# Kernel tuning notes

Measured on AMD Instinct MI355X. Metric: run time of the kernel, lower is better.

## Reference

```python
import jax, jax.numpy as jnp
import numpy as np

IN_F, OUT_F, R = 4096, 4096, 16
SCALING = 32.0 / R  # lora_alpha / r


def setup_inputs() -> dict:
    key = jax.random.key(0)
    kx, kw, kb, ka, kB = jax.random.split(key, 5)
    bound_w = 1.0 / np.sqrt(IN_F)  # kaiming_uniform a=sqrt(5) on (out,in) -> U(-1/sqrt(in), 1/sqrt(in))
    x = jax.random.normal(kx, (4, 4096, IN_F), dtype=jnp.float32)
    weight = jax.random.uniform(kw, (OUT_F, IN_F), jnp.float32, -bound_w, bound_w)
    bias = jax.random.uniform(kb, (OUT_F,), jnp.float32, -bound_w, bound_w)
    lora_A = jax.random.uniform(ka, (R, IN_F), jnp.float32, -bound_w, bound_w)
    # B is zero-init in the module; use small random values so the LoRA path is exercised
    lora_B = jax.random.normal(kB, (OUT_F, R), dtype=jnp.float32) * 0.01
    return {"x": x, "weight": weight, "bias": bias, "lora_A": lora_A, "lora_B": lora_B}


def reference(x, weight, bias, lora_A, lora_B):
    # base: F.linear(x, W, b) = x @ W.T + b
    base_out = jnp.einsum("bsi,oi->bso", x, weight) + bias
    # low-rank path: (x @ A.T) @ B.T * scaling  (dropout=0 -> identity)
    xr = jnp.einsum("bsi,ri->bsr", x, lora_A)  # [b, s, r]
    lora_out = jnp.einsum("bsr,or->bso", xr, lora_B) * SCALING
    return base_out + lora_out
```

## Files before the change

### kernel.cpp

```cpp
#include <hip/hip_runtime.h>
#include <hip/hip_bf16.h>


typedef __attribute__((ext_vector_type(8))) short bf16x8;
typedef __attribute__((ext_vector_type(4))) float f32x4;
typedef __attribute__((ext_vector_type(4))) unsigned short u16x4;

#define M_DIM 16384
#define N_DIM 4096
#define K_DIM 4096
#define NT (K_DIM / 64)

__device__ __forceinline__ unsigned short f2bf(float f) {
    unsigned int u = __builtin_bit_cast(unsigned int, f);
    unsigned int r = u + 0x7FFFu + ((u >> 16) & 1u);
    return (unsigned short)(r >> 16);
}

__device__ __forceinline__ void async16(const void* g, void* l) {
    __builtin_amdgcn_global_load_lds(
        (const __attribute__((address_space(1))) unsigned int*)g,
        (__attribute__((address_space(3))) unsigned int*)l,
        16, 0, 0);
}

__global__ void __launch_bounds__(256) cast_x_kernel(
    const float4* __restrict__ x, u16x4* __restrict__ y, int n4) {
    int i = blockIdx.x * blockDim.x + threadIdx.x;
    int stride = gridDim.x * blockDim.x;
    for (; i < n4; i += stride) {
        float4 v = x[i];
        u16x4 o = { f2bf(v.x), f2bf(v.y), f2bf(v.z), f2bf(v.w) };
        y[i] = o;
    }
}

__global__ void __launch_bounds__(256) weff_kernel(
    const float* __restrict__ W, const float* __restrict__ lA,
    const float* __restrict__ lB, unsigned short* __restrict__ out) {
    constexpr int K = K_DIM, R = 16;
    constexpr float S = 2.0f;
    int o = blockIdx.x;
    int t = threadIdx.x;
    float b[R];
#pragma unroll
    for (int r = 0; r < R; ++r) b[r] = lB[o * R + r];
#pragma unroll
    for (int c = 0; c < 4; ++c) {
        int i = c * 1024 + t * 4;
        float4 wv = *reinterpret_cast<const float4*>(&W[o * K + i]);
        float sx = 0.f, sy = 0.f, sz = 0.f, sw = 0.f;
#pragma unroll
        for (int r = 0; r < R; ++r) {
            float4 a = *reinterpret_cast<const float4*>(&lA[r * K + i]);
            sx += b[r] * a.x; sy += b[r] * a.y;
            sz += b[r] * a.z; sw += b[r] * a.w;
        }
        u16x4 ov = { f2bf(wv.x + S * sx), f2bf(wv.y + S * sy),
                     f2bf(wv.z + S * sz), f2bf(wv.w + S * sw) };
        *reinterpret_cast<u16x4*>(&out[o * K + i]) = ov;
    }
}

#define STAGE(G, h, tt, bsel, moff)                                           \
    do {                                                                      \
        const unsigned short* g0 = (G) +                                      \
            (size_t)((h) * 128 + wid * 16 + rc) * K_DIM + (tt) * 64 + cc * 8; \
        char* l0 = lds + (bsel) * 65536 + (moff) + (h) * 16384 + wid * 2048;  \
        async16(g0, l0);                                                      \
        async16(g0 + 8 * K_DIM, l0 + 1024);                                   \
    } while (0)

#define LDA(mh, bsel)                                                         \
    _Pragma("unroll") for (int mm = 0; mm < 4; ++mm)                          \
    _Pragma("unroll") for (int ks = 0; ks < 2; ++ks)                          \
        ar[mm][ks] = *(const bf16x8*)(lds + (bsel) * 65536 +                  \
            ((aBase + ((mh) * 4 + mm) * 2048) ^ (ks << 6)));

#define LDB(nh, bsel)                                                         \
    _Pragma("unroll") for (int nn = 0; nn < 2; ++nn)                          \
    _Pragma("unroll") for (int ks = 0; ks < 2; ++ks)                          \
        br[(nh) * 2 + nn][ks] = *(const bf16x8*)(lds + (bsel) * 65536 +       \
            ((bBase + ((nh) * 2 + nn) * 2048) ^ (ks << 6)));

#define MM(mh, nh)                                                            \
    _Pragma("unroll") for (int ks = 0; ks < 2; ++ks)                          \
    _Pragma("unroll") for (int mm = 0; mm < 4; ++mm)                          \
    _Pragma("unroll") for (int nn = 0; nn < 2; ++nn)                          \
        acc[(mh) * 4 + mm][(nh) * 2 + nn] =                                   \
            __builtin_amdgcn_mfma_f32_16x16x32_bf16(                          \
                ar[mm][ks], br[(nh) * 2 + nn][ks],                            \
                acc[(mh) * 4 + mm][(nh) * 2 + nn], 0, 0, 0);

#define PHASE_MID()                                                           \
    __builtin_amdgcn_s_barrier();                                             \
    asm volatile("s_waitcnt lgkmcnt(0)" ::: "memory");                        \
    __builtin_amdgcn_s_setprio(1)

#define PHASE_END()                                                           \
    __builtin_amdgcn_s_setprio(0);                                            \
    __builtin_amdgcn_s_barrier()

__global__ void __launch_bounds__(512, 2) gemm8p_kernel(
    const unsigned short* __restrict__ A,
    const unsigned short* __restrict__ B,
    const float* __restrict__ bias,
    float* __restrict__ C) {
    __shared__ __align__(1024) char lds[131072];

    const int tid = threadIdx.x;
    const int lane = tid & 63, wid = tid >> 6;
    const int wm = wid >> 2, wn = wid & 3;
    const int lr = lane & 15, lg = lane >> 4;

    const int bid = blockIdx.x;
    const int swz = (bid & 7) * 128 + (bid >> 3);
    const int bm = swz >> 4, bn = swz & 15;

    const unsigned short* Ag = A + (size_t)bm * 256 * K_DIM;
    const unsigned short* Bg = B + (size_t)bn * 256 * K_DIM;

    const int lam = lane ^ (lane >> 3);
    const int rc = lam >> 3, cc = lam & 7;

    const int kx0 = (lg * 16) ^ ((lr & 7) << 4);
    const int aBase = (wm * 128 + lr) * 128 + kx0;
    const int bBase = 32768 + (wn * 64 + lr) * 128 + kx0;

    f32x4 acc[8][4] = {};
    bf16x8 ar[4][2], br[4][2];

    STAGE(Bg, 0, 0, 0, 32768);
    STAGE(Bg, 1, 0, 0, 32768);
    STAGE(Ag, 0, 0, 0, 0);
    STAGE(Ag, 1, 0, 0, 0);
    STAGE(Bg, 0, 1, 1, 32768);
    STAGE(Bg, 1, 1, 1, 32768);
    asm volatile("s_waitcnt vmcnt(4)" ::: "memory");
    __builtin_amdgcn_s_barrier();

#pragma unroll 2
    for (int t = 0; t < NT; ++t) {
        const int bs = t & 1, bo = bs ^ 1;
        LDA(0, bs);
        LDB(0, bs);
        if (t + 1 < NT) STAGE(Ag, 0, t + 1, bo, 0);
        PHASE_MID();
        MM(0, 0);
        PHASE_END();
        LDB(1, bs);
        if (t + 1 < NT) STAGE(Ag, 1, t + 1, bo, 0);
        PHASE_MID();
        MM(0, 1);
        PHASE_END();
        LDA(1, bs);
        if (t + 2 < NT) STAGE(Bg, 0, t + 2, bs, 32768);
        PHASE_MID();
        MM(1, 0);
        PHASE_END();
        if (t + 2 < NT) STAGE(Bg, 1, t + 2, bs, 32768);
        PHASE_MID();
        MM(1, 1);
        __builtin_amdgcn_s_setprio(0);
        if (t + 2 < NT) {
            asm volatile("s_waitcnt vmcnt(4)" ::: "memory");
        } else {
            asm volatile("s_waitcnt vmcnt(0)" ::: "memory");
        }
        __builtin_amdgcn_s_barrier();
    }

    const int row0 = bm * 256 + wm * 128;
    const int col0 = bn * 256 + wn * 64;
#pragma unroll
    for (int n = 0; n < 4; ++n) {
        const int col = col0 + n * 16 + lr;
        const float bv = bias[col];
#pragma unroll
        for (int m = 0; m < 8; ++m) {
            const int r0 = row0 + m * 16 + lg * 4;
#pragma unroll
            for (int r = 0; r < 4; ++r)
                C[(size_t)(r0 + r) * N_DIM + col] = acc[m][n][r] + bv;
        }
    }
}

extern "C" void kernel_launch(void* const* d_in, const int* in_sizes, int n_in,
                              void* d_out, int out_size, void* d_ws, size_t ws_size,
                              hipStream_t stream) {
    const float* x    = (const float*)d_in[0];
    const float* W    = (const float*)d_in[1];
    const float* bias = (const float*)d_in[2];
    const float* lA   = (const float*)d_in[3];
    const float* lB   = (const float*)d_in[4];
    float* out = (float*)d_out;

    unsigned short* xb   = (unsigned short*)d_ws;
    unsigned short* weff = (unsigned short*)((char*)d_ws + 134217728);

    cast_x_kernel<<<2048, 256, 0, stream>>>((const float4*)x, (u16x4*)xb,
                                            M_DIM * K_DIM / 4);
    weff_kernel<<<N_DIM, 256, 0, stream>>>(W, lA, lB, weff);
    gemm8p_kernel<<<(M_DIM / 256) * (N_DIM / 256), 512, 0, stream>>>(
        xb, weff, bias, out);
}
```

Measured before the change: 604.4 us.

## Switch GEMM inner loop to 32x32x16 bf16 MFMA and drop phase barriers

Replaces the 16x16x32 MFMA tiling with 32x32x16 bf16 MFMA instructions. Each wave now holds 4x2 tiles of 32x32 accumulators, and LDS fragment loads and swizzle offsets are recomputed for the new operand layout. Larger MFMA tiles need fewer LDS reads per flop and fewer instructions. Two of the four per-phase end barriers are also removed, cutting synchronisation. The trade-off is higher register pressure and a different LDS access pattern, and the reduced barriers could risk races on buffer reuse.

```diff
diff --git a/kernel.cpp b/kernel.cpp
--- a/kernel.cpp
+++ b/kernel.cpp
@@ -3,7 +3,7 @@
 
 
 typedef __attribute__((ext_vector_type(8))) short bf16x8;
-typedef __attribute__((ext_vector_type(4))) float f32x4;
+typedef __attribute__((ext_vector_type(16))) float f32x16;
 typedef __attribute__((ext_vector_type(4))) unsigned short u16x4;
 
 #define M_DIM 16384
@@ -71,35 +71,27 @@
         async16(g0 + 8 * K_DIM, l0 + 1024);                                   \
     } while (0)
 
-#define LDA(mh, bsel)                                                         \
-    _Pragma("unroll") for (int mm = 0; mm < 4; ++mm)                          \
-    _Pragma("unroll") for (int ks = 0; ks < 2; ++ks)                          \
-        ar[mm][ks] = *(const bf16x8*)(lds + (bsel) * 65536 +                  \
-            ((aBase + ((mh) * 4 + mm) * 2048) ^ (ks << 6)));
-
-#define LDB(nh, bsel)                                                         \
-    _Pragma("unroll") for (int nn = 0; nn < 2; ++nn)                          \
-    _Pragma("unroll") for (int ks = 0; ks < 2; ++ks)                          \
-        br[(nh) * 2 + nn][ks] = *(const bf16x8*)(lds + (bsel) * 65536 +       \
-            ((bBase + ((nh) * 2 + nn) * 2048) ^ (ks << 6)));
-
-#define MM(mh, nh)                                                            \
-    _Pragma("unroll") for (int ks = 0; ks < 2; ++ks)                          \
-    _Pragma("unroll") for (int mm = 0; mm < 4; ++mm)                          \
-    _Pragma("unroll") for (int nn = 0; nn < 2; ++nn)                          \
-        acc[(mh) * 4 + mm][(nh) * 2 + nn] =                                   \
-            __builtin_amdgcn_mfma_f32_16x16x32_bf16(                          \
-                ar[mm][ks], br[(nh) * 2 + nn][ks],                            \
-                acc[(mh) * 4 + mm][(nh) * 2 + nn], 0, 0, 0);
+#define LDA32(mh, bsel)                                                       \
+    _Pragma("unroll") for (int mm = 0; mm < 2; ++mm)                          \
+    _Pragma("unroll") for (int ks = 0; ks < 4; ++ks)                          \
+        ar[mm][ks] = *(const bf16x8*)(lds + (bsel) * 65536 + aoff +           \
+            ((mh) * 2 + mm) * 4096 + kx[ks]);
+
+#define LDB32(nh, bsel)                                                       \
+    _Pragma("unroll") for (int ks = 0; ks < 4; ++ks)                          \
+        br[nh][ks] = *(const bf16x8*)(lds + (bsel) * 65536 + boff +           \
+            (nh) * 4096 + kx[ks]);
+
+#define MM32(mh, nh)                                                          \
+    _Pragma("unroll") for (int ks = 0; ks < 4; ++ks)                          \
+    _Pragma("unroll") for (int mm = 0; mm < 2; ++mm)                          \
+        acc[(mh) * 2 + mm][nh] = __builtin_amdgcn_mfma_f32_32x32x16_bf16(     \
+            ar[mm][ks], br[nh][ks], acc[(mh) * 2 + mm][nh], 0, 0, 0);
 
 #define PHASE_MID()                                                           \
     __builtin_amdgcn_s_barrier();                                             \
     asm volatile("s_waitcnt lgkmcnt(0)" ::: "memory");                        \
     __builtin_amdgcn_s_setprio(1)
-
-#define PHASE_END()                                                           \
-    __builtin_amdgcn_s_setprio(0);                                            \
-    __builtin_amdgcn_s_barrier()
 
 __global__ void __launch_bounds__(512, 2) gemm8p_kernel(
     const unsigned short* __restrict__ A,
@@ -111,7 +103,7 @@
     const int tid = threadIdx.x;
     const int lane = tid & 63, wid = tid >> 6;
     const int wm = wid >> 2, wn = wid & 3;
-    const int lr = lane & 15, lg = lane >> 4;
+    const int lc = lane & 31, hi = lane >> 5;
 
     const int bid = blockIdx.x;
     const int swz = (bid & 7) * 128 + (bid >> 3);
@@ -123,12 +115,15 @@
     const int lam = lane ^ (lane >> 3);
     const int rc = lam >> 3, cc = lam & 7;
 
-    const int kx0 = (lg * 16) ^ ((lr & 7) << 4);
-    const int aBase = (wm * 128 + lr) * 128 + kx0;
-    const int bBase = 32768 + (wn * 64 + lr) * 128 + kx0;
-
-    f32x4 acc[8][4] = {};
-    bf16x8 ar[4][2], br[4][2];
+    const int sw = (lane & 7) << 4;
+    int kx[4];
+#pragma unroll
+    for (int ks = 0; ks < 4; ++ks) kx[ks] = ((ks << 5) | (hi << 4)) ^ sw;
+    const int aoff = (wm * 128 + lc) * 128;
+    const int boff = 32768 + (wn * 64 + lc) * 128;
+
+    f32x16 acc[4][2] = {};
+    bf16x8 ar[2][4], br[2][4];
 
     STAGE(Bg, 0, 0, 0, 32768);
     STAGE(Bg, 1, 0, 0, 32768);
@@ -142,25 +137,26 @@
 #pragma unroll 2
     for (int t = 0; t < NT; ++t) {
         const int bs = t & 1, bo = bs ^ 1;
-        LDA(0, bs);
-        LDB(0, bs);
+        LDA32(0, bs);
+        LDB32(0, bs);
         if (t + 1 < NT) STAGE(Ag, 0, t + 1, bo, 0);
         PHASE_MID();
-        MM(0, 0);
-        PHASE_END();
-        LDB(1, bs);
+        MM32(0, 0);
+        __builtin_amdgcn_s_setprio(0);
+        LDB32(1, bs);
         if (t + 1 < NT) STAGE(Ag, 1, t + 1, bo, 0);
         PHASE_MID();
-        MM(0, 1);
-        PHASE_END();
-        LDA(1, bs);
+        MM32(0, 1);
+        __builtin_amdgcn_s_setprio(0);
+        __builtin_amdgcn_s_barrier();
+        LDA32(1, bs);
         if (t + 2 < NT) STAGE(Bg, 0, t + 2, bs, 32768);
         PHASE_MID();
-        MM(1, 0);
-        PHASE_END();
+        MM32(1, 0);
+        __builtin_amdgcn_s_setprio(0);
         if (t + 2 < NT) STAGE(Bg, 1, t + 2, bs, 32768);
         PHASE_MID();
-        MM(1, 1);
+        MM32(1, 1);
         __builtin_amdgcn_s_setprio(0);
         if (t + 2 < NT) {
             asm volatile("s_waitcnt vmcnt(4)" ::: "memory");
@@ -173,15 +169,19 @@
     const int row0 = bm * 256 + wm * 128;
     const int col0 = bn * 256 + wn * 64;
 #pragma unroll
-    for (int n = 0; n < 4; ++n) {
-        const int col = col0 + n * 16 + lr;
+    for (int n = 0; n < 2; ++n) {
+        const int col = col0 + n * 32 + lc;
         const float bv = bias[col];
 #pragma unroll
-        for (int m = 0; m < 8; ++m) {
-            const int r0 = row0 + m * 16 + lg * 4;
-#pragma unroll
-            for (int r = 0; r < 4; ++r)
-                C[(size_t)(r0 + r) * N_DIM + col] = acc[m][n][r] + bv;
+        for (int m = 0; m < 4; ++m) {
+#pragma unroll
+            for (int g = 0; g < 4; ++g) {
+#pragma unroll
+                for (int r = 0; r < 4; ++r) {
+                    const int row = row0 + m * 32 + g * 8 + 4 * hi + r;
+                    C[(size_t)row * N_DIM + col] = acc[m][n][g * 4 + r] + bv;
+                }
+            }
         }
     }
 }
```

Result: slower. 643.8 us (+6.5%).

## Make GEMM persistent over four tiles with cross-tile prefetch and fewer barriers

Applied to the files above, without the earlier changes.

The GEMM grid shrinks from 1024 blocks to 256, and each block walks a 2x2 group of 256x256 output tiles in a snake order. Loads for the next tile are issued during the last iterations of the current tile, so the pipeline does not drain and refill between tiles. Two of the four per-iteration barriers are also removed. The intent is to cut per-block prologue/epilogue cost, tail imbalance and barrier overhead. The risks are a single wave of 256 blocks leaving some CUs idle and races from the removed barriers.

```diff
diff --git a/kernel.cpp b/kernel.cpp
--- a/kernel.cpp
+++ b/kernel.cpp
@@ -9,7 +9,7 @@
 #define M_DIM 16384
 #define N_DIM 4096
 #define K_DIM 4096
-#define NT (K_DIM / 64)
+#define NT 64
 
 __device__ __forceinline__ unsigned short f2bf(float f) {
     unsigned int u = __builtin_bit_cast(unsigned int, f);
@@ -97,10 +97,6 @@
     asm volatile("s_waitcnt lgkmcnt(0)" ::: "memory");                        \
     __builtin_amdgcn_s_setprio(1)
 
-#define PHASE_END()                                                           \
-    __builtin_amdgcn_s_setprio(0);                                            \
-    __builtin_amdgcn_s_barrier()
-
 __global__ void __launch_bounds__(512, 2) gemm8p_kernel(
     const unsigned short* __restrict__ A,
     const unsigned short* __restrict__ B,
@@ -114,11 +110,16 @@
     const int lr = lane & 15, lg = lane >> 4;
 
     const int bid = blockIdx.x;
-    const int swz = (bid & 7) * 128 + (bid >> 3);
-    const int bm = swz >> 4, bn = swz & 15;
-
-    const unsigned short* Ag = A + (size_t)bm * 256 * K_DIM;
-    const unsigned short* Bg = B + (size_t)bn * 256 * K_DIM;
+    const int qm = bid >> 3, qn = bid & 7;
+    const int bmArr[4] = { 2 * qm, 2 * qm, 2 * qm + 1, 2 * qm + 1 };
+    const int bnArr[4] = { 2 * qn, 2 * qn + 1, 2 * qn + 1, 2 * qn };
+    const unsigned short* AgArr[4];
+    const unsigned short* BgArr[4];
+#pragma unroll
+    for (int i = 0; i < 4; ++i) {
+        AgArr[i] = A + (size_t)bmArr[i] * 256 * K_DIM;
+        BgArr[i] = B + (size_t)bnArr[i] * 256 * K_DIM;
+    }
 
     const int lam = lane ^ (lane >> 3);
     const int rc = lam >> 3, cc = lam & 7;
@@ -127,61 +128,78 @@
     const int aBase = (wm * 128 + lr) * 128 + kx0;
     const int bBase = 32768 + (wn * 64 + lr) * 128 + kx0;
 
-    f32x4 acc[8][4] = {};
     bf16x8 ar[4][2], br[4][2];
 
-    STAGE(Bg, 0, 0, 0, 32768);
-    STAGE(Bg, 1, 0, 0, 32768);
-    STAGE(Ag, 0, 0, 0, 0);
-    STAGE(Ag, 1, 0, 0, 0);
-    STAGE(Bg, 0, 1, 1, 32768);
-    STAGE(Bg, 1, 1, 1, 32768);
+    STAGE(BgArr[0], 0, 0, 0, 32768);
+    STAGE(BgArr[0], 1, 0, 0, 32768);
+    STAGE(AgArr[0], 0, 0, 0, 0);
+    STAGE(AgArr[0], 1, 0, 0, 0);
+    STAGE(BgArr[0], 0, 1, 1, 32768);
+    STAGE(BgArr[0], 1, 1, 1, 32768);
     asm volatile("s_waitcnt vmcnt(4)" ::: "memory");
     __builtin_amdgcn_s_barrier();
 
+#pragma unroll
+    for (int tau = 0; tau < 4; ++tau) {
+        const int nx = (tau < 3) ? tau + 1 : 3;
+        const unsigned short* AgC = AgArr[tau];
+        const unsigned short* AgN = AgArr[nx];
+        const unsigned short* BgC = BgArr[tau];
+        const unsigned short* BgN = BgArr[nx];
+
+        f32x4 acc[8][4] = {};
+
 #pragma unroll 2
-    for (int t = 0; t < NT; ++t) {
-        const int bs = t & 1, bo = bs ^ 1;
-        LDA(0, bs);
-        LDB(0, bs);
-        if (t + 1 < NT) STAGE(Ag, 0, t + 1, bo, 0);
-        PHASE_MID();
-        MM(0, 0);
-        PHASE_END();
-        LDB(1, bs);
-        if (t + 1 < NT) STAGE(Ag, 1, t + 1, bo, 0);
-        PHASE_MID();
-        MM(0, 1);
-        PHASE_END();
-        LDA(1, bs);
-        if (t + 2 < NT) STAGE(Bg, 0, t + 2, bs, 32768);
-        PHASE_MID();
-        MM(1, 0);
-        PHASE_END();
-        if (t + 2 < NT) STAGE(Bg, 1, t + 2, bs, 32768);
-        PHASE_MID();
-        MM(1, 1);
-        __builtin_amdgcn_s_setprio(0);
-        if (t + 2 < NT) {
-            asm volatile("s_waitcnt vmcnt(4)" ::: "memory");
-        } else {
-            asm volatile("s_waitcnt vmcnt(0)" ::: "memory");
+        for (int t = 0; t < NT; ++t) {
+            const int bs = t & 1, bo = bs ^ 1;
+            const unsigned short* As = (t < NT - 1) ? AgC : AgN;
+            const unsigned short* Bs = (t < NT - 2) ? BgC : BgN;
+            const int ta = (t + 1) & 63;
+            const int tb = (t + 2) & 63;
+            const bool doA = (tau < 3) || (t < NT - 1);
+            const bool doB = (tau < 3) || (t < NT - 2);
+            LDA(0, bs);
+            LDB(0, bs);
+            if (doA) STAGE(As, 0, ta, bo, 0);
+            PHASE_MID();
+            MM(0, 0);
+            __builtin_amdgcn_s_setprio(0);
+            LDB(1, bs);
+            if (doA) STAGE(As, 1, ta, bo, 0);
+            PHASE_MID();
+            MM(0, 1);
+            __builtin_amdgcn_s_setprio(0);
+            __builtin_amdgcn_s_barrier();
+            LDA(1, bs);
+            if (doB) STAGE(Bs, 0, tb, bs, 32768);
+            PHASE_MID();
+            MM(1, 0);
+            __builtin_amdgcn_s_setprio(0);
+            if (doB) STAGE(Bs, 1, tb, bs, 32768);
+            PHASE_MID();
+            MM(1, 1);
+            __builtin_amdgcn_s_setprio(0);
+            if (doB) {
+                asm volatile("s_waitcnt vmcnt(4)" ::: "memory");
+            } else {
+                asm volatile("s_waitcnt vmcnt(0)" ::: "memory");
+            }
+            __builtin_amdgcn_s_barrier();
         }
-        __builtin_amdgcn_s_barrier();
-    }
-
-    const int row0 = bm * 256 + wm * 128;
-    const int col0 = bn * 256 + wn * 64;
-#pragma unroll
-    for (int n = 0; n < 4; ++n) {
-        const int col = col0 + n * 16 + lr;
-        const float bv = bias[col];
-#pragma unroll
-        for (int m = 0; m < 8; ++m) {
-            const int r0 = row0 + m * 16 + lg * 4;
-#pragma unroll
-            for (int r = 0; r < 4; ++r)
-                C[(size_t)(r0 + r) * N_DIM + col] = acc[m][n][r] + bv;
+
+        const int row0 = bmArr[tau] * 256 + wm * 128;
+        const int col0 = bnArr[tau] * 256 + wn * 64;
+#pragma unroll
+        for (int n = 0; n < 4; ++n) {
+            const int col = col0 + n * 16 + lr;
+            const float bv = bias[col];
+#pragma unroll
+            for (int m = 0; m < 8; ++m) {
+                const int r0 = row0 + m * 16 + lg * 4;
+#pragma unroll
+                for (int r = 0; r < 4; ++r)
+                    C[(size_t)(r0 + r) * N_DIM + col] = acc[m][n][r] + bv;
+            }
         }
     }
 }
@@ -202,6 +220,5 @@
     cast_x_kernel<<<2048, 256, 0, stream>>>((const float4*)x, (u16x4*)xb,
                                             M_DIM * K_DIM / 4);
     weff_kernel<<<N_DIM, 256, 0, stream>>>(W, lA, lB, weff);
-    gemm8p_kernel<<<(M_DIM / 256) * (N_DIM / 256), 512, 0, stream>>>(
-        xb, weff, bias, out);
-}
+    gemm8p_kernel<<<256, 512, 0, stream>>>(xb, weff, bias, out);
+}
```

After: 682.3 us. 12.9% more time.

## Cut GEMM main-loop barriers from eight to two with double-buffered A fragments

Applied to the files above, without the earlier changes.

Restructures the bf16 GEMM inner loop so that all B fragments and the first A half are loaded up front, both A-tile async stages are issued together, and the second A half goes into a separate register set while the first MFMA quarter runs. This removes most of the per-phase barriers and explicit lgkmcnt waits, leaving one mid-loop barrier and one end barrier per iteration, with MFMA priority raised around each quarter. The aim is to cut synchronisation stalls and let LDS reads overlap MFMA work. In exchange it uses more registers, and it relies on compiler-inserted waits to keep the async B refill from overwriting LDS that is still being read.

```diff
diff --git a/kernel.cpp b/kernel.cpp
--- a/kernel.cpp
+++ b/kernel.cpp
@@ -9,7 +9,7 @@
 #define M_DIM 16384
 #define N_DIM 4096
 #define K_DIM 4096
-#define NT (K_DIM / 64)
+#define NT 64
 
 __device__ __forceinline__ unsigned short f2bf(float f) {
     unsigned int u = __builtin_bit_cast(unsigned int, f);
@@ -71,37 +71,32 @@
         async16(g0 + 8 * K_DIM, l0 + 1024);                                   \
     } while (0)
 
-#define LDA(mh, bsel)                                                         \
+#define LDA_TO(dst, mh, bsel)                                                 \
     _Pragma("unroll") for (int mm = 0; mm < 4; ++mm)                          \
     _Pragma("unroll") for (int ks = 0; ks < 2; ++ks)                          \
-        ar[mm][ks] = *(const bf16x8*)(lds + (bsel) * 65536 +                  \
+        dst[mm][ks] = *(const bf16x8*)(lds + (bsel) * 65536 +                 \
             ((aBase + ((mh) * 4 + mm) * 2048) ^ (ks << 6)));
 
-#define LDB(nh, bsel)                                                         \
+#define LDB_TO(nh, bsel)                                                      \
     _Pragma("unroll") for (int nn = 0; nn < 2; ++nn)                          \
     _Pragma("unroll") for (int ks = 0; ks < 2; ++ks)                          \
         br[(nh) * 2 + nn][ks] = *(const bf16x8*)(lds + (bsel) * 65536 +       \
             ((bBase + ((nh) * 2 + nn) * 2048) ^ (ks << 6)));
 
-#define MM(mh, nh)                                                            \
+#define MM_Q(src, mh, nh)                                                     \
+    __builtin_amdgcn_s_setprio(1);                                            \
     _Pragma("unroll") for (int ks = 0; ks < 2; ++ks)                          \
     _Pragma("unroll") for (int mm = 0; mm < 4; ++mm)                          \
     _Pragma("unroll") for (int nn = 0; nn < 2; ++nn)                          \
         acc[(mh) * 4 + mm][(nh) * 2 + nn] =                                   \
             __builtin_amdgcn_mfma_f32_16x16x32_bf16(                          \
-                ar[mm][ks], br[(nh) * 2 + nn][ks],                            \
-                acc[(mh) * 4 + mm][(nh) * 2 + nn], 0, 0, 0);
-
-#define PHASE_MID()                                                           \
-    __builtin_amdgcn_s_barrier();                                             \
-    asm volatile("s_waitcnt lgkmcnt(0)" ::: "memory");                        \
-    __builtin_amdgcn_s_setprio(1)
-
-#define PHASE_END()                                                           \
-    __builtin_amdgcn_s_setprio(0);                                            \
-    __builtin_amdgcn_s_barrier()
-
-__global__ void __launch_bounds__(512, 2) gemm8p_kernel(
+                src[mm][ks], br[(nh) * 2 + nn][ks],                           \
+                acc[(mh) * 4 + mm][(nh) * 2 + nn], 0, 0, 0);                  \
+    __builtin_amdgcn_s_setprio(0)
+
+#define CFENCE() asm volatile("" ::: "memory")
+
+__global__ void __launch_bounds__(512, 2) gemm2b_kernel(
     const unsigned short* __restrict__ A,
     const unsigned short* __restrict__ B,
     const float* __restrict__ bias,
@@ -128,7 +123,7 @@
     const int bBase = 32768 + (wn * 64 + lr) * 128 + kx0;
 
     f32x4 acc[8][4] = {};
-    bf16x8 ar[4][2], br[4][2];
+    bf16x8 arA[4][2], arB[4][2], br[4][2];
 
     STAGE(Bg, 0, 0, 0, 32768);
     STAGE(Bg, 1, 0, 0, 32768);
@@ -138,36 +133,35 @@
     STAGE(Bg, 1, 1, 1, 32768);
     asm volatile("s_waitcnt vmcnt(4)" ::: "memory");
     __builtin_amdgcn_s_barrier();
+    CFENCE();
 
 #pragma unroll 2
     for (int t = 0; t < NT; ++t) {
         const int bs = t & 1, bo = bs ^ 1;
-        LDA(0, bs);
-        LDB(0, bs);
-        if (t + 1 < NT) STAGE(Ag, 0, t + 1, bo, 0);
-        PHASE_MID();
-        MM(0, 0);
-        PHASE_END();
-        LDB(1, bs);
-        if (t + 1 < NT) STAGE(Ag, 1, t + 1, bo, 0);
-        PHASE_MID();
-        MM(0, 1);
-        PHASE_END();
-        LDA(1, bs);
+        LDA_TO(arA, 0, bs);
+        LDB_TO(0, bs);
+        LDB_TO(1, bs);
+        if (t + 1 < NT) {
+            STAGE(Ag, 0, t + 1, bo, 0);
+            STAGE(Ag, 1, t + 1, bo, 0);
+        }
+        MM_Q(arA, 0, 0);
+        LDA_TO(arB, 1, bs);
+        MM_Q(arA, 0, 1);
+        CFENCE();
+        __builtin_amdgcn_s_barrier();
+        CFENCE();
         if (t + 2 < NT) STAGE(Bg, 0, t + 2, bs, 32768);
-        PHASE_MID();
-        MM(1, 0);
-        PHASE_END();
+        MM_Q(arB, 1, 0);
         if (t + 2 < NT) STAGE(Bg, 1, t + 2, bs, 32768);
-        PHASE_MID();
-        MM(1, 1);
-        __builtin_amdgcn_s_setprio(0);
-        if (t + 2 < NT) {
+        MM_Q(arB, 1, 1);
+        if (t < NT - 2) {
             asm volatile("s_waitcnt vmcnt(4)" ::: "memory");
         } else {
             asm volatile("s_waitcnt vmcnt(0)" ::: "memory");
         }
         __builtin_amdgcn_s_barrier();
+        CFENCE();
     }
 
     const int row0 = bm * 256 + wm * 128;
@@ -202,6 +196,6 @@
     cast_x_kernel<<<2048, 256, 0, stream>>>((const float4*)x, (u16x4*)xb,
                                             M_DIM * K_DIM / 4);
     weff_kernel<<<N_DIM, 256, 0, stream>>>(W, lA, lB, weff);
-    gemm8p_kernel<<<(M_DIM / 256) * (N_DIM / 256), 512, 0, stream>>>(
+    gemm2b_kernel<<<(M_DIM / 256) * (N_DIM / 256), 512, 0, stream>>>(
         xb, weff, bias, out);
 }
```

After: 590.5 us. 2.3% less time.
